# Optimization experiments

Measured on AMD Instinct MI355X. Metric: run time of the kernel, lower is better.

The kernel has to match this reference:

```python
import jax, jax.numpy as jnp
import numpy as np

B, S, DX, DH = 8, 4096, 512, 512


def log_g(x):
    # log of g(x) where g(x) = relu(x)+0.5 for x>=0 and sigmoid-like for x<0
    return jnp.where(x >= 0, jnp.log(jax.nn.relu(x) + 0.5), -jax.nn.softplus(-x))


def parallel_scan(log_coeffs, log_values):
    # log_coeffs: (B, S, H); log_values: (B, S+1, H)
    # Heinsen log-space linear-recurrence scan.
    a_star = jnp.pad(jnp.cumsum(log_coeffs, axis=1), ((0, 0), (1, 0), (0, 0)))  # (B,S+1,H)
    log_h = a_star + jax.lax.cumlogsumexp(log_values - a_star, axis=1)
    return log_h[:, 1:]  # (B, S, H)


def setup_inputs() -> dict:
    key = jax.random.key(0)
    ks = jax.random.split(key, 8)
    sx = 1.0 / np.sqrt(DX)
    sh = 1.0 / np.sqrt(DH)
    return {
        "x": jax.random.normal(ks[0], (B, S, DX), dtype=jnp.float32),
        "h_prev": jax.random.uniform(ks[1], (B, 1, DH), dtype=jnp.float32),
        "Wz": jax.random.uniform(ks[2], (DX, DH), jnp.float32, -sx, sx),
        "bz": jax.random.uniform(ks[3], (DH,), jnp.float32, -sx, sx),
        "Wh": jax.random.uniform(ks[4], (DX, DH), jnp.float32, -sx, sx),
        "bh": jax.random.uniform(ks[5], (DH,), jnp.float32, -sx, sx),
        "Wo": jax.random.uniform(ks[6], (DH, DX), jnp.float32, -sh, sh),
        "bo": jax.random.uniform(ks[7], (DX,), jnp.float32, -sh, sh),
    }


def reference(x, h_prev, Wz, bz, Wh, bh, Wo, bo):
    k = jnp.einsum('bsd,dh->bsh', x, Wz) + bz           # gate pre-activation
    tilde_h = jnp.einsum('bsd,dh->bsh', x, Wh) + bh     # candidate hidden
    log_z = -jax.nn.softplus(-k)
    log_one_minus_z = -jax.nn.softplus(k)
    log_h_prev = log_g(h_prev)                          # (B,1,H)
    log_tilde_h = log_g(tilde_h)                        # (B,S,H)
    log_vals = jnp.concatenate([log_h_prev, log_z + log_tilde_h], axis=1)  # (B,S+1,H)
    log_h = parallel_scan(log_one_minus_z, log_vals)    # (B,S,H)
    h = jnp.exp(log_h)
    out = jnp.einsum('bsh,hd->bsd', h, Wo) + bo         # (B,S,DX)
    return out
```

## Files before the change

kernel.cpp:

```cpp
#include <hip/hip_runtime.h>


using bf16x8 = __attribute__((ext_vector_type(8))) short;
using f32x4  = __attribute__((ext_vector_type(4))) float;

#define NB 8
#define NS 4096
#define ND 512
#define MR (NB*NS)
#define SC 128
#define WU 64
#define NCHUNK (NS/SC)

__device__ __forceinline__ unsigned short f2bf(float f) {
  unsigned u = __float_as_uint(f);
  u += 0x7fffu + ((u >> 16) & 1u);
  return (unsigned short)(u >> 16);
}

__device__ __forceinline__ void gload16(const void* g, void* l) {
  __builtin_amdgcn_global_load_lds(
      (const __attribute__((address_space(1))) void*)g,
      (__attribute__((address_space(3))) void*)l, 16, 0, 0);
}

__global__ void prep_x_kernel(const float4* __restrict__ x4, ushort4* __restrict__ xb4, int n4) {
  for (int i = blockIdx.x * blockDim.x + threadIdx.x; i < n4; i += gridDim.x * blockDim.x) {
    float4 f = x4[i];
    ushort4 o;
    o.x = f2bf(f.x); o.y = f2bf(f.y); o.z = f2bf(f.z); o.w = f2bf(f.w);
    xb4[i] = o;
  }
}

__global__ void prep_w_kernel(const float* __restrict__ Wz, const float* __restrict__ Wh,
                              const float* __restrict__ Wo,
                              unsigned short* __restrict__ WzhT, unsigned short* __restrict__ WoT) {
  int i = blockIdx.x * blockDim.x + threadIdx.x;
  if (i < 1024 * 512) {
    int n = i >> 9, kk = i & 511;
    int g = n >> 6, w = n & 63;
    int h = g * 32 + (w & 31);
    float val = (w < 32) ? Wz[kk * 512 + h] : Wh[kk * 512 + h];
    WzhT[i] = f2bf(val);
  } else if (i < 1024 * 512 + 512 * 512) {
    int j = i - 1024 * 512;
    int d = j >> 9, hh = j & 511;
    WoT[j] = f2bf(Wo[hh * 512 + d]);
  }
}

__device__ __forceinline__ void gemm_core(const unsigned short* __restrict__ A,
                                          const unsigned short* __restrict__ Bt,
                                          int m0, int n0,
                                          unsigned short* As, unsigned short* Bs,
                                          f32x4 (&acc)[4][4]) {
  const int tid  = threadIdx.x;
  const int lane = tid & 63;
  const int wave = tid >> 6;
  const int wm = wave & 1, wn = wave >> 1;

  const f32x4 zero = {0.f, 0.f, 0.f, 0.f};
#pragma unroll
  for (int m = 0; m < 4; ++m)
#pragma unroll
    for (int n = 0; n < 4; ++n) acc[m][n] = zero;

  for (int kt = 0; kt < 512; kt += 64) {
#pragma unroll
    for (int it = 0; it < 4; ++it) {
      int flat = it * 256 + tid;
      int row = flat >> 3, c16 = flat & 7;
      int srcb = (c16 * 16) ^ ((row & 7) << 4);
      gload16(A  + (size_t)(m0 + row) * 512 + kt + (srcb >> 1),
              As + (it * 256 + wave * 64) * 8);
      gload16(Bt + (size_t)(n0 + row) * 512 + kt + (srcb >> 1),
              Bs + (it * 256 + wave * 64) * 8);
    }
    __syncthreads();
#pragma unroll
    for (int ks = 0; ks < 2; ++ks) {
      bf16x8 af[4], bfr[4];
#pragma unroll
      for (int m = 0; m < 4; ++m) {
        int row = wm * 64 + m * 16 + (lane & 15);
        int kb  = ks * 64 + ((lane >> 4) << 4);
        af[m] = *(const bf16x8*)((const char*)As + row * 128 + (kb ^ ((row & 7) << 4)));
      }
#pragma unroll
      for (int n = 0; n < 4; ++n) {
        int row = wn * 64 + n * 16 + (lane & 15);
        int kb  = ks * 64 + ((lane >> 4) << 4);
        bfr[n] = *(const bf16x8*)((const char*)Bs + row * 128 + (kb ^ ((row & 7) << 4)));
      }
#pragma unroll
      for (int m = 0; m < 4; ++m)
#pragma unroll
        for (int n = 0; n < 4; ++n)
          acc[m][n] = __builtin_amdgcn_mfma_f32_16x16x32_bf16(af[m], bfr[n], acc[m][n], 0, 0, 0);
    }
    __syncthreads();
  }
}

__global__ __launch_bounds__(256) void gemm1_kernel(const unsigned short* __restrict__ xb,
                                                    const unsigned short* __restrict__ WzhT,
                                                    const float* __restrict__ bz,
                                                    const float* __restrict__ bh,
                                                    unsigned int* __restrict__ cv) {
  __shared__ unsigned short As[128 * 64];
  __shared__ unsigned short Bs[128 * 64];
  int bid = blockIdx.x;
  int nt = bid & 7, mt = bid >> 3;
  int m0 = mt * 128, n0 = nt * 128;
  f32x4 acc[4][4];
  gemm_core(xb, WzhT, m0, n0, As, Bs, acc);

  const int lane = threadIdx.x & 63;
  const int wave = threadIdx.x >> 6;
  const int wm = wave & 1, wn = wave >> 1;
  int g = nt * 2 + wn;
#pragma unroll
  for (int n = 0; n < 2; ++n) {
    int h = g * 32 + n * 16 + (lane & 15);
    float bzv = bz[h], bhv = bh[h];
#pragma unroll
    for (int m = 0; m < 4; ++m) {
#pragma unroll
      for (int r = 0; r < 4; ++r) {
        int rowg = m0 + wm * 64 + m * 16 + ((lane >> 4) << 2) + r;
        float kv = acc[m][n][r]     + bzv;
        float tv = acc[m][n + 2][r] + bhv;
        float z  = 1.f / (1.f + __expf(-kv));
        float c  = 1.f / (1.f + __expf(kv));
        float gg = (tv >= 0.f) ? (tv + 0.5f) : (1.f / (1.f + __expf(-tv)));
        float vv = z * gg;
        cv[(size_t)rowg * 512 + h] = ((unsigned)f2bf(vv) << 16) | (unsigned)f2bf(c);
      }
    }
  }
}

__global__ __launch_bounds__(512) void scan_kernel(const unsigned int* __restrict__ cv,
                                                   const float* __restrict__ hprev,
                                                   unsigned short* __restrict__ hbuf) {
  int b = blockIdx.x >> 5;
  int chunk = blockIdx.x & 31;
  int h = threadIdx.x;
  int s0 = chunk * SC;
  float acc;
  int sstart;
  if (chunk == 0) {
    float hp = hprev[b * 512 + h];
    acc = (hp >= 0.f) ? (hp + 0.5f) : (1.f / (1.f + __expf(-hp)));
    sstart = 0;
  } else {
    acc = 0.f;
    sstart = s0 - WU;
  }
  const unsigned int* p = cv + ((size_t)(b * NS + sstart) << 9) + h;
  for (int s = sstart; s < s0; s += 8) {
    unsigned int u[8];
#pragma unroll
    for (int j = 0; j < 8; ++j) u[j] = p[(size_t)j << 9];
    p += (size_t)8 << 9;
#pragma unroll
    for (int j = 0; j < 8; ++j)
      acc = fmaf(__uint_as_float(u[j] << 16), acc, __uint_as_float(u[j] & 0xffff0000u));
  }
  unsigned short* q = hbuf + ((size_t)(b * NS + s0) << 9) + h;
  for (int s = 0; s < SC; s += 8) {
    unsigned int u[8];
#pragma unroll
    for (int j = 0; j < 8; ++j) u[j] = p[(size_t)j << 9];
    p += (size_t)8 << 9;
#pragma unroll
    for (int j = 0; j < 8; ++j) {
      acc = fmaf(__uint_as_float(u[j] << 16), acc, __uint_as_float(u[j] & 0xffff0000u));
      q[(size_t)j << 9] = f2bf(acc);
    }
    q += (size_t)8 << 9;
  }
}

__global__ __launch_bounds__(256) void gemm2_kernel(const unsigned short* __restrict__ hb,
                                                    const unsigned short* __restrict__ WoT,
                                                    const float* __restrict__ bo,
                                                    float* __restrict__ out) {
  __shared__ unsigned short As[128 * 64];
  __shared__ unsigned short Bs[128 * 64];
  int bid = blockIdx.x;
  int nt = bid & 3, mt = bid >> 2;
  int m0 = mt * 128, n0 = nt * 128;
  f32x4 acc[4][4];
  gemm_core(hb, WoT, m0, n0, As, Bs, acc);

  const int lane = threadIdx.x & 63;
  const int wave = threadIdx.x >> 6;
  const int wm = wave & 1, wn = wave >> 1;
#pragma unroll
  for (int n = 0; n < 4; ++n) {
    int colg = n0 + wn * 64 + n * 16 + (lane & 15);
    float bov = bo[colg];
#pragma unroll
    for (int m = 0; m < 4; ++m) {
#pragma unroll
      for (int r = 0; r < 4; ++r) {
        int rowg = m0 + wm * 64 + m * 16 + ((lane >> 4) << 2) + r;
        out[(size_t)rowg * 512 + colg] = acc[m][n][r] + bov;
      }
    }
  }
}

extern "C" void kernel_launch(void* const* d_in, const int* in_sizes, int n_in,
                              void* d_out, int out_size, void* d_ws, size_t ws_size,
                              hipStream_t stream) {
  const float* x     = (const float*)d_in[0];
  const float* hprev = (const float*)d_in[1];
  const float* Wz    = (const float*)d_in[2];
  const float* bz    = (const float*)d_in[3];
  const float* Wh    = (const float*)d_in[4];
  const float* bh    = (const float*)d_in[5];
  const float* Wo    = (const float*)d_in[6];
  const float* bo    = (const float*)d_in[7];
  float* out = (float*)d_out;

  char* ws = (char*)d_ws;
  unsigned short* xb   = (unsigned short*)(ws);
  unsigned short* hbuf = (unsigned short*)(ws);
  unsigned short* WzhT = (unsigned short*)(ws + ((size_t)32 << 20));
  unsigned short* WoT  = (unsigned short*)(ws + ((size_t)33 << 20));
  unsigned int* cv = (unsigned int*)d_out;

  prep_x_kernel<<<2048, 256, 0, stream>>>((const float4*)x, (ushort4*)xb, (NB * NS * ND) / 4);
  prep_w_kernel<<<3072, 256, 0, stream>>>(Wz, Wh, Wo, WzhT, WoT);
  gemm1_kernel<<<2048, 256, 0, stream>>>(xb, WzhT, bz, bh, cv);
  scan_kernel<<<NB * NCHUNK, 512, 0, stream>>>(cv, hprev, hbuf);
  gemm2_kernel<<<1024, 256, 0, stream>>>(hbuf, WoT, bo, out);
}
```

Measured before the change: 248.6 us.

## Double-buffer GEMM LDS tiles, remap blocks across XCDs, halve scan chunk size

The GEMM main loop now uses two LDS buffers, so the global-to-LDS load for the next K tile is issued before computing the current one. This overlaps memory latency with MFMA work and cuts one barrier per iteration, at the cost of doubled LDS per block. Block IDs are remapped so that consecutive blocks, which are dispatched round-robin to different XCDs, handle neighbouring M tiles, likely to improve per-XCD L2 reuse of A rows. The scan chunk size is halved to 64, doubling the number of scan blocks for more parallelism. Each chunk still carries a 64-step warm-up, so total scan reads grow.

```diff
diff --git a/kernel.cpp b/kernel.cpp
--- a/kernel.cpp
+++ b/kernel.cpp
@@ -7,8 +7,7 @@
 #define NB 8
 #define NS 4096
 #define ND 512
-#define MR (NB*NS)
-#define SC 128
+#define SC 64
 #define WU 64
 #define NCHUNK (NS/SC)
 
@@ -50,10 +49,52 @@
   }
 }
 
+__device__ __forceinline__ void stage_tile(const unsigned short* __restrict__ A,
+                                           const unsigned short* __restrict__ Bt,
+                                           int m0, int n0, int kt, int tid, int wave,
+                                           unsigned short* As, unsigned short* Bs) {
+#pragma unroll
+  for (int it = 0; it < 4; ++it) {
+    int flat = it * 256 + tid;
+    int row = flat >> 3, c16 = flat & 7;
+    int srcb = (c16 * 16) ^ ((row & 7) << 4);
+    gload16(A  + (size_t)(m0 + row) * 512 + kt + (srcb >> 1),
+            As + (it * 256 + wave * 64) * 8);
+    gload16(Bt + (size_t)(n0 + row) * 512 + kt + (srcb >> 1),
+            Bs + (it * 256 + wave * 64) * 8);
+  }
+}
+
+__device__ __forceinline__ void compute_tile(const unsigned short* As, const unsigned short* Bs,
+                                             int lane, int wm, int wn, f32x4 (&acc)[4][4]) {
+#pragma unroll
+  for (int ks = 0; ks < 2; ++ks) {
+    bf16x8 af[4], bfr[4];
+#pragma unroll
+    for (int m = 0; m < 4; ++m) {
+      int row = wm * 64 + m * 16 + (lane & 15);
+      int kb  = ks * 64 + ((lane >> 4) << 4);
+      af[m] = *(const bf16x8*)((const char*)As + row * 128 + (kb ^ ((row & 7) << 4)));
+    }
+#pragma unroll
+    for (int n = 0; n < 4; ++n) {
+      int row = wn * 64 + n * 16 + (lane & 15);
+      int kb  = ks * 64 + ((lane >> 4) << 4);
+      bfr[n] = *(const bf16x8*)((const char*)Bs + row * 128 + (kb ^ ((row & 7) << 4)));
+    }
+#pragma unroll
+    for (int m = 0; m < 4; ++m)
+#pragma unroll
+      for (int n = 0; n < 4; ++n)
+        acc[m][n] = __builtin_amdgcn_mfma_f32_16x16x32_bf16(af[m], bfr[n], acc[m][n], 0, 0, 0);
+  }
+}
+
 __device__ __forceinline__ void gemm_core(const unsigned short* __restrict__ A,
                                           const unsigned short* __restrict__ Bt,
                                           int m0, int n0,
-                                          unsigned short* As, unsigned short* Bs,
+                                          unsigned short (&As)[2][128 * 64],
+                                          unsigned short (&Bs)[2][128 * 64],
                                           f32x4 (&acc)[4][4]) {
   const int tid  = threadIdx.x;
   const int lane = tid & 63;
@@ -66,41 +107,16 @@
 #pragma unroll
     for (int n = 0; n < 4; ++n) acc[m][n] = zero;
 
-  for (int kt = 0; kt < 512; kt += 64) {
-#pragma unroll
-    for (int it = 0; it < 4; ++it) {
-      int flat = it * 256 + tid;
-      int row = flat >> 3, c16 = flat & 7;
-      int srcb = (c16 * 16) ^ ((row & 7) << 4);
-      gload16(A  + (size_t)(m0 + row) * 512 + kt + (srcb >> 1),
-              As + (it * 256 + wave * 64) * 8);
-      gload16(Bt + (size_t)(n0 + row) * 512 + kt + (srcb >> 1),
-              Bs + (it * 256 + wave * 64) * 8);
-    }
+  stage_tile(A, Bt, m0, n0, 0, tid, wave, As[0], Bs[0]);
+  __syncthreads();
+#pragma unroll
+  for (int t = 0; t < 7; ++t) {
+    const int cur = t & 1;
+    stage_tile(A, Bt, m0, n0, (t + 1) * 64, tid, wave, As[cur ^ 1], Bs[cur ^ 1]);
+    compute_tile(As[cur], Bs[cur], lane, wm, wn, acc);
     __syncthreads();
-#pragma unroll
-    for (int ks = 0; ks < 2; ++ks) {
-      bf16x8 af[4], bfr[4];
-#pragma unroll
-      for (int m = 0; m < 4; ++m) {
-        int row = wm * 64 + m * 16 + (lane & 15);
-        int kb  = ks * 64 + ((lane >> 4) << 4);
-        af[m] = *(const bf16x8*)((const char*)As + row * 128 + (kb ^ ((row & 7) << 4)));
-      }
-#pragma unroll
-      for (int n = 0; n < 4; ++n) {
-        int row = wn * 64 + n * 16 + (lane & 15);
-        int kb  = ks * 64 + ((lane >> 4) << 4);
-        bfr[n] = *(const bf16x8*)((const char*)Bs + row * 128 + (kb ^ ((row & 7) << 4)));
-      }
-#pragma unroll
-      for (int m = 0; m < 4; ++m)
-#pragma unroll
-        for (int n = 0; n < 4; ++n)
-          acc[m][n] = __builtin_amdgcn_mfma_f32_16x16x32_bf16(af[m], bfr[n], acc[m][n], 0, 0, 0);
-    }
-    __syncthreads();
-  }
+  }
+  compute_tile(As[1], Bs[1], lane, wm, wn, acc);
 }
 
 __global__ __launch_bounds__(256) void gemm1_kernel(const unsigned short* __restrict__ xb,
@@ -108,10 +124,12 @@
                                                     const float* __restrict__ bz,
                                                     const float* __restrict__ bh,
                                                     unsigned int* __restrict__ cv) {
-  __shared__ unsigned short As[128 * 64];
-  __shared__ unsigned short Bs[128 * 64];
+  __shared__ unsigned short As[2][128 * 64];
+  __shared__ unsigned short Bs[2][128 * 64];
   int bid = blockIdx.x;
-  int nt = bid & 7, mt = bid >> 3;
+  int x = bid & 7, i = bid >> 3;
+  int nt = i & 7;
+  int mt = x + ((i >> 3) << 3);
   int m0 = mt * 128, n0 = nt * 128;
   f32x4 acc[4][4];
   gemm_core(xb, WzhT, m0, n0, As, Bs, acc);
@@ -144,8 +162,8 @@
 __global__ __launch_bounds__(512) void scan_kernel(const unsigned int* __restrict__ cv,
                                                    const float* __restrict__ hprev,
                                                    unsigned short* __restrict__ hbuf) {
-  int b = blockIdx.x >> 5;
-  int chunk = blockIdx.x & 31;
+  int b = blockIdx.x >> 6;
+  int chunk = blockIdx.x & 63;
   int h = threadIdx.x;
   int s0 = chunk * SC;
   float acc;
@@ -187,10 +205,12 @@
                                                     const unsigned short* __restrict__ WoT,
                                                     const float* __restrict__ bo,
                                                     float* __restrict__ out) {
-  __shared__ unsigned short As[128 * 64];
-  __shared__ unsigned short Bs[128 * 64];
+  __shared__ unsigned short As[2][128 * 64];
+  __shared__ unsigned short Bs[2][128 * 64];
   int bid = blockIdx.x;
-  int nt = bid & 3, mt = bid >> 2;
+  int x = bid & 7, i = bid >> 3;
+  int nt = i & 3;
+  int mt = x + ((i >> 2) << 3);
   int m0 = mt * 128, n0 = nt * 128;
   f32x4 acc[4][4];
   gemm_core(hb, WoT, m0, n0, As, Bs, acc);
```

Measured after the change: 236.6 us. -4.9%, faster.
